# Kernel tuning notes

Measured on AMD Instinct MI355X. Metric: run time of the kernel, lower is better.

## Reference

```python
import jax, jax.numpy as jnp
import numpy as np
from jax import lax

H = 64  # hidden size


def _lstm_layer(x, w_ih, w_hh, b_ih, b_hh):
    """Single LSTM layer, batch_first x: [B, T, D] -> [B, T, H].
    PyTorch gate order: i, f, g, o."""
    B = x.shape[0]
    # Precompute input projections for all timesteps: [T, B, 4H]
    xg = jnp.einsum('btd,gd->tbg', x, w_ih) + (b_ih + b_hh)

    def step(carry, xg_t):
        h, c = carry
        gates = xg_t + h @ w_hh.T  # [B, 4H]
        i, f, g, o = jnp.split(gates, 4, axis=-1)
        i = jax.nn.sigmoid(i)
        f = jax.nn.sigmoid(f)
        g = jnp.tanh(g)
        o = jax.nn.sigmoid(o)
        c = f * c + i * g
        h = o * jnp.tanh(c)
        return (h, c), h

    h0 = jnp.zeros((B, H), dtype=x.dtype)
    c0 = jnp.zeros((B, H), dtype=x.dtype)
    (_, _), hs = lax.scan(step, (h0, c0), xg)  # hs: [T, B, H]
    return jnp.swapaxes(hs, 0, 1)  # [B, T, H]


def setup_inputs() -> dict:
    key = jax.random.key(0)
    ks = jax.random.split(key, 11)
    s = 1.0 / np.sqrt(H)  # PyTorch LSTM init scale
    x = jax.random.normal(ks[0], (8192, 168, 7), dtype=jnp.float32)
    return {
        'x': x,
        'w_ih0': jax.random.normal(ks[1], (4 * H, 7), jnp.float32) * s,
        'w_hh0': jax.random.normal(ks[2], (4 * H, H), jnp.float32) * s,
        'b_ih0': jax.random.normal(ks[3], (4 * H,), jnp.float32) * s,
        'b_hh0': jax.random.normal(ks[4], (4 * H,), jnp.float32) * s,
        'w_ih1': jax.random.normal(ks[5], (4 * H, H), jnp.float32) * s,
        'w_hh1': jax.random.normal(ks[6], (4 * H, H), jnp.float32) * s,
        'b_ih1': jax.random.normal(ks[7], (4 * H,), jnp.float32) * s,
        'b_hh1': jax.random.normal(ks[8], (4 * H,), jnp.float32) * s,
        'fc_w': jax.random.normal(ks[9], (4, H), jnp.float32) * s,
        'fc_b': jax.random.normal(ks[10], (4,), jnp.float32) * s,
    }


def reference(x, w_ih0, w_hh0, b_ih0, b_hh0, w_ih1, w_hh1, b_ih1, b_hh1, fc_w, fc_b):
    h1 = _lstm_layer(x, w_ih0, w_hh0, b_ih0, b_hh0)   # [B, T, H]
    h2 = _lstm_layer(h1, w_ih1, w_hh1, b_ih1, b_hh1)  # [B, T, H]
    last = h2[:, -1, :]                               # dropout is identity in eval
    return last @ fc_w.T + fc_b                       # [B, 4]
```

## Files before the change

kernel.cpp:

```cpp
#include <hip/hip_runtime.h>

#define TT 168
#define HH 64
#define DD 7
#define NS 16
#define BB 8192
#define CH 8
#define NTH 512

typedef float f32x4 __attribute__((ext_vector_type(4)));
typedef _Float16 f16x8 __attribute__((ext_vector_type(8)));

#define MFMA16F(A, B, C) __builtin_amdgcn_mfma_f32_16x16x32_f16((A), (B), (C), 0, 0, 0)

__device__ __forceinline__ f16x8 pack8(f32x4 a, f32x4 b) {
    f16x8 r;
#pragma unroll
    for (int e = 0; e < 4; ++e) { r[e] = (_Float16)a[e]; r[4 + e] = (_Float16)b[e]; }
    return r;
}

__device__ __forceinline__ void cell_update(const f32x4& si, const f32x4& sf,
                                            const f32x4& sg, const f32x4& so,
                                            f32x4& cst, _Float16* dst) {
    f32x4 hv;
#pragma unroll
    for (int r = 0; r < 4; ++r) {
        const float uf = __builtin_amdgcn_exp2f(sf[r]);
        const float fv = __builtin_amdgcn_rcpf(1.0f + uf);
        const float ui = __builtin_amdgcn_exp2f(si[r]);
        const float ug = __builtin_amdgcn_exp2f(fminf(sg[r], 80.0f));
        const float R1 = __builtin_amdgcn_rcpf((1.0f + ui) * (1.0f + ug));
        const float ig = (1.0f - ug) * R1;
        cst[r] = fv * cst[r] + ig;
        const float uo = __builtin_amdgcn_exp2f(so[r]);
        const float uc = __builtin_amdgcn_exp2f(fminf(cst[r] * -2.88539008f, 80.0f));
        const float R2 = __builtin_amdgcn_rcpf((1.0f + uo) * (1.0f + uc));
        hv[r] = (1.0f - uc) * R2;
    }
    unsigned d0, d1;
    asm("v_cvt_pkrtz_f16_f32 %0, %1, %2" : "=v"(d0) : "v"(hv[0]), "v"(hv[1]));
    asm("v_cvt_pkrtz_f16_f32 %0, %1, %2" : "=v"(d1) : "v"(hv[2]), "v"(hv[3]));
    *(uint2*)dst = make_uint2(d0, d1);
}

__global__ __launch_bounds__(NTH, 4)
void weather_lstm_mfma(const float* __restrict__ x,
                       const float* __restrict__ w_ih0, const float* __restrict__ w_hh0,
                       const float* __restrict__ b_ih0, const float* __restrict__ b_hh0,
                       const float* __restrict__ w_ih1, const float* __restrict__ w_hh1,
                       const float* __restrict__ b_ih1, const float* __restrict__ b_hh1,
                       const float* __restrict__ fc_w, const float* __restrict__ fc_b,
                       float* __restrict__ out)
{
    __shared__ f16x8 xs[2][CH][NS];
    __shared__ __align__(16) _Float16 h1[2][NS][72];
    __shared__ __align__(16) _Float16 h2[2][NS][72];

    const int tid  = threadIdx.x;
    const int wv   = tid >> 6;
    const int q    = wv & 3;
    const int lane = tid & 63;
    const int col  = lane & 15;
    const int kg   = lane >> 4;
    const int s0   = blockIdx.x * NS;
    const int ub   = 16 * q + 4 * kg;

    for (int i = tid; i < 2 * NS * 72; i += NTH) {
        ((short*)h1)[i] = 0; ((short*)h2)[i] = 0;
    }
    if (tid < CH * NS) {
        const int tloc = tid >> 4, ss = tid & 15;
        const float* px = x + ((size_t)(s0 + ss) * TT + tloc) * DD;
        f32x4 a, b;
        a[0] = px[0]; a[1] = px[1]; a[2] = px[2]; a[3] = px[3];
        b[0] = px[4]; b[1] = px[5]; b[2] = px[6]; b[3] = 1.0f;
        xs[0][tloc][ss] = pack8(a, b);
    }
    __syncthreads();

    const f16x8 z8 = {0, 0, 0, 0, 0, 0, 0, 0};
    const f32x4 zz = {0, 0, 0, 0};

    if (wv < 4) {
        f16x8 W0[4][2], WX[4];
#pragma unroll
        for (int t4 = 0; t4 < 4; ++t4) {
            const float sc = (t4 == 2) ? -2.88539008f : -1.44269504f;
            const int row = 64 * t4 + 16 * q + col;
#pragma unroll
            for (int kf = 0; kf < 2; ++kf) {
                const float* p = w_hh0 + (size_t)row * HH + 32 * kf + 8 * kg;
                W0[t4][kf] = pack8(*(const f32x4*)p * sc, *(const f32x4*)(p + 4) * sc);
            }
            f32x4 a = {0, 0, 0, 0}, b = {0, 0, 0, 0};
            if (kg == 0) {
                const float* p = w_ih0 + (size_t)row * DD;
                a[0] = p[0]; a[1] = p[1]; a[2] = p[2]; a[3] = p[3];
                b[0] = p[4]; b[1] = p[5]; b[2] = p[6];
                b[3] = b_ih0[row] + b_hh0[row];
            }
            WX[t4] = pack8(a * sc, b * sc);
        }
        f32x4 c1 = {0, 0, 0, 0};

        const f16x8* xbase = &xs[0][0][0];
        const _Float16* r0a = &h1[0][col][8 * kg];
        const _Float16* r0b = &h1[0][col][32 + 8 * kg];
        const _Float16* r1a = &h1[1][col][8 * kg];
        const _Float16* r1b = &h1[1][col][32 + 8 * kg];
        _Float16* wp0 = &h1[0][col][ub];
        _Float16* wp1 = &h1[1][col][ub];

        auto l0_step = [&](const f16x8* xp, const _Float16* ra, const _Float16* rb,
                           _Float16* wr) {
            f32x4 a0, a1, a2, a3;
            __builtin_amdgcn_s_setprio(1);
            f16x8 ax = z8;
            if (kg == 0) ax = *xp;
            a0 = MFMA16F(WX[0], ax, zz);
            a1 = MFMA16F(WX[1], ax, zz);
            a2 = MFMA16F(WX[2], ax, zz);
            a3 = MFMA16F(WX[3], ax, zz);
            f16x8 dh = *(const f16x8*)ra;
            a0 = MFMA16F(W0[0][0], dh, a0);
            a1 = MFMA16F(W0[1][0], dh, a1);
            a2 = MFMA16F(W0[2][0], dh, a2);
            a3 = MFMA16F(W0[3][0], dh, a3);
            dh = *(const f16x8*)rb;
            a0 = MFMA16F(W0[0][1], dh, a0);
            a1 = MFMA16F(W0[1][1], dh, a1);
            a2 = MFMA16F(W0[2][1], dh, a2);
            a3 = MFMA16F(W0[3][1], dh, a3);
            __builtin_amdgcn_s_setprio(0);
            cell_update(a0, a1, a2, a3, c1, wr);
        };
        auto refill = [&](int kref) {
            if (tid < CH * NS) {
                const int tloc = tid >> 4, ss = tid & 15;
                const int tg = kref + CH + tloc;
                const float* px = x + ((size_t)(s0 + ss) * TT + tg) * DD;
                f32x4 a, b;
                a[0] = px[0]; a[1] = px[1]; a[2] = px[2]; a[3] = px[3];
                b[0] = px[4]; b[1] = px[5]; b[2] = px[6]; b[3] = 1.0f;
                const int nb = ((kref >> 3) & 1) ^ 1;
                xs[nb][tloc][ss] = pack8(a, b);
            }
        };

        refill(0);
        l0_step(xbase + col, r1a, r1b, wp0);
        __syncthreads();
        l0_step(xbase + NS + col, r0a, r0b, wp1);
        __syncthreads();

#pragma unroll 1
        for (int j = 1; j < 84; ++j) {
            const f16x8* xpA = xbase + ((2 * j) & 15) * NS + col;
            if ((j & 3) == 0 && j < 80) refill(2 * j);
            l0_step(xpA, r1a, r1b, wp0);
            __syncthreads();
            l0_step(xpA + NS, r0a, r0b, wp1);
            __syncthreads();
        }
        __syncthreads();
    } else {
        f16x8 W1[4][4];
        f32x4 bias1[4];
#pragma unroll
        for (int t4 = 0; t4 < 4; ++t4) {
            const float sc = (t4 == 2) ? -2.88539008f : -1.44269504f;
            const int row = 64 * t4 + 16 * q + col;
            const int rr  = 64 * t4 + 16 * q + 4 * kg;
            bias1[t4] = (*(const f32x4*)(b_ih1 + rr) + *(const f32x4*)(b_hh1 + rr)) * sc;
#pragma unroll
            for (int kf = 0; kf < 4; ++kf) {
                const float* base = (kf < 2) ? (w_ih1 + (size_t)row * HH + 32 * kf)
                                             : (w_hh1 + (size_t)row * HH + 32 * (kf - 2));
                const float* p = base + 8 * kg;
                W1[t4][kf] = pack8(*(const f32x4*)p * sc, *(const f32x4*)(p + 4) * sc);
            }
        }
        f32x4 c2 = {0, 0, 0, 0};

        const _Float16* p1a0 = &h1[0][col][8 * kg];
        const _Float16* p1b0 = &h1[0][col][32 + 8 * kg];
        const _Float16* p1a1 = &h1[1][col][8 * kg];
        const _Float16* p1b1 = &h1[1][col][32 + 8 * kg];
        const _Float16* p2a0 = &h2[0][col][8 * kg];
        const _Float16* p2b0 = &h2[0][col][32 + 8 * kg];
        const _Float16* p2a1 = &h2[1][col][8 * kg];
        const _Float16* p2b1 = &h2[1][col][32 + 8 * kg];
        _Float16* q0 = &h2[0][col][ub];
        _Float16* q1 = &h2[1][col][ub];

        auto l1_step = [&](const _Float16* ha, const _Float16* hb,
                           const _Float16* ea, const _Float16* eb, _Float16* wr) {
            f32x4 a0, a1, a2, a3;
            __builtin_amdgcn_s_setprio(1);
            f16x8 dh = *(const f16x8*)ha;
            a0 = MFMA16F(W1[0][0], dh, bias1[0]);
            a1 = MFMA16F(W1[1][0], dh, bias1[1]);
            a2 = MFMA16F(W1[2][0], dh, bias1[2]);
            a3 = MFMA16F(W1[3][0], dh, bias1[3]);
            dh = *(const f16x8*)hb;
            a0 = MFMA16F(W1[0][1], dh, a0);
            a1 = MFMA16F(W1[1][1], dh, a1);
            a2 = MFMA16F(W1[2][1], dh, a2);
            a3 = MFMA16F(W1[3][1], dh, a3);
            dh = *(const f16x8*)ea;
            a0 = MFMA16F(W1[0][2], dh, a0);
            a1 = MFMA16F(W1[1][2], dh, a1);
            a2 = MFMA16F(W1[2][2], dh, a2);
            a3 = MFMA16F(W1[3][2], dh, a3);
            dh = *(const f16x8*)eb;
            a0 = MFMA16F(W1[0][3], dh, a0);
            a1 = MFMA16F(W1[1][3], dh, a1);
            a2 = MFMA16F(W1[2][3], dh, a2);
            a3 = MFMA16F(W1[3][3], dh, a3);
            __builtin_amdgcn_s_setprio(0);
            cell_update(a0, a1, a2, a3, c2, wr);
        };

        __syncthreads();
        l1_step(p1a0, p1b0, p2a1, p2b1, q0);
        __syncthreads();

#pragma unroll 1
        for (int j = 1; j < 84; ++j) {
            l1_step(p1a1, p1b1, p2a0, p2b0, q1);
            __syncthreads();
            l1_step(p1a0, p1b0, p2a1, p2b1, q0);
            __syncthreads();
        }
        l1_step(p1a1, p1b1, p2a0, p2b0, q1);
        __syncthreads();
    }

    if (tid < NS * 4) {
        const int s = tid >> 2, k = tid & 3;
        float a = fc_b[k];
#pragma unroll
        for (int j = 0; j < HH; ++j)
            a = fmaf((float)h2[1][s][j], fc_w[k * HH + j], a);
        out[(size_t)(s0 + s) * 4 + k] = a;
    }
}

extern "C" void kernel_launch(void* const* d_in, const int* in_sizes, int n_in,
                              void* d_out, int out_size, void* d_ws, size_t ws_size,
                              hipStream_t stream) {
    const float* x     = (const float*)d_in[0];
    const float* w_ih0 = (const float*)d_in[1];
    const float* w_hh0 = (const float*)d_in[2];
    const float* b_ih0 = (const float*)d_in[3];
    const float* b_hh0 = (const float*)d_in[4];
    const float* w_ih1 = (const float*)d_in[5];
    const float* w_hh1 = (const float*)d_in[6];
    const float* b_ih1 = (const float*)d_in[7];
    const float* b_hh1 = (const float*)d_in[8];
    const float* fc_w  = (const float*)d_in[9];
    const float* fc_b  = (const float*)d_in[10];
    float* out = (float*)d_out;

    dim3 grid(BB / NS), block(NTH);
    weather_lstm_mfma<<<grid, block, 0, stream>>>(
        x, w_ih0, w_hh0, b_ih0, b_hh0,
        w_ih1, w_hh1, b_ih1, b_hh1, fc_w, fc_b, out);
}
```

Baseline: 228.2 us.

## Pair cell updates with packed math, drop setprio, zero-padded x buffer

Rewrites the LSTM cell nonlinearity to process two elements at a time with float2 vectors, which permits packed-math instructions. It also merges the forget and input gate reciprocals into one rcp by sharing a denominator, and stores c in a pre-scaled form. The x staging buffer gets a per-kg zero-padded slot so every lane loads unconditionally instead of branching on kg==0. The s_setprio calls around the MFMA sections are removed. The shared-denominator product can overflow or lose precision for large gate inputs, even with exp clamped at 40.

```diff
diff --git a/kernel.cpp b/kernel.cpp
--- a/kernel.cpp
+++ b/kernel.cpp
@@ -8,6 +8,7 @@
 #define CH 8
 #define NTH 512
 
+typedef float f32x2 __attribute__((ext_vector_type(2)));
 typedef float f32x4 __attribute__((ext_vector_type(4)));
 typedef _Float16 f16x8 __attribute__((ext_vector_type(8)));
 
@@ -20,27 +21,43 @@
     return r;
 }
 
-__device__ __forceinline__ void cell_update(const f32x4& si, const f32x4& sf,
-                                            const f32x4& sg, const f32x4& so,
-                                            f32x4& cst, _Float16* dst) {
-    f32x4 hv;
-#pragma unroll
-    for (int r = 0; r < 4; ++r) {
-        const float uf = __builtin_amdgcn_exp2f(sf[r]);
-        const float fv = __builtin_amdgcn_rcpf(1.0f + uf);
-        const float ui = __builtin_amdgcn_exp2f(si[r]);
-        const float ug = __builtin_amdgcn_exp2f(fminf(sg[r], 80.0f));
-        const float R1 = __builtin_amdgcn_rcpf((1.0f + ui) * (1.0f + ug));
-        const float ig = (1.0f - ug) * R1;
-        cst[r] = fv * cst[r] + ig;
-        const float uo = __builtin_amdgcn_exp2f(so[r]);
-        const float uc = __builtin_amdgcn_exp2f(fminf(cst[r] * -2.88539008f, 80.0f));
-        const float R2 = __builtin_amdgcn_rcpf((1.0f + uo) * (1.0f + uc));
-        hv[r] = (1.0f - uc) * R2;
-    }
+__device__ __forceinline__ f32x2 exp2x2(f32x2 a) {
+    return (f32x2){__builtin_amdgcn_exp2f(fminf(a.x, 40.0f)),
+                   __builtin_amdgcn_exp2f(fminf(a.y, 40.0f))};
+}
+__device__ __forceinline__ f32x2 rcpx2(f32x2 a) {
+    return (f32x2){__builtin_amdgcn_rcpf(a.x), __builtin_amdgcn_rcpf(a.y)};
+}
+
+__device__ __forceinline__ void cell_pair(f32x2 si, f32x2 sf, f32x2 sg, f32x2 so,
+                                          f32x2& cs, unsigned& dpk) {
+    const f32x2 one = {1.0f, 1.0f};
+    const f32x2 ui  = exp2x2(si);
+    const f32x2 uf  = exp2x2(sf);
+    const f32x2 ug  = exp2x2(sg);
+    const f32x2 opf = one + uf;
+    const f32x2 pig = (one + ui) * (one + ug);
+    const f32x2 R1  = rcpx2(pig * opf);
+    const f32x2 fv  = pig * R1;
+    const f32x2 igs = (ug * 2.88539008f - (f32x2){2.88539008f, 2.88539008f}) * (opf * R1);
+    cs = fv * cs + igs;
+    const f32x2 uo = exp2x2(so);
+    const f32x2 uc = exp2x2(cs);
+    const f32x2 R2 = rcpx2((one + uo) * (one + uc));
+    const f32x2 hv = (one - uc) * R2;
+    asm("v_cvt_pkrtz_f16_f32 %0, %1, %2" : "=v"(dpk) : "v"(hv.x), "v"(hv.y));
+}
+
+__device__ __forceinline__ void cell_update(const f32x4& gi, const f32x4& gf,
+                                            const f32x4& gg, const f32x4& go,
+                                            f32x4& cs, _Float16* dst) {
+    f32x2 csA = {cs[0], cs[1]}, csB = {cs[2], cs[3]};
     unsigned d0, d1;
-    asm("v_cvt_pkrtz_f16_f32 %0, %1, %2" : "=v"(d0) : "v"(hv[0]), "v"(hv[1]));
-    asm("v_cvt_pkrtz_f16_f32 %0, %1, %2" : "=v"(d1) : "v"(hv[2]), "v"(hv[3]));
+    cell_pair((f32x2){gi[0], gi[1]}, (f32x2){gf[0], gf[1]},
+              (f32x2){gg[0], gg[1]}, (f32x2){go[0], go[1]}, csA, d0);
+    cell_pair((f32x2){gi[2], gi[3]}, (f32x2){gf[2], gf[3]},
+              (f32x2){gg[2], gg[3]}, (f32x2){go[2], go[3]}, csB, d1);
+    cs[0] = csA.x; cs[1] = csA.y; cs[2] = csB.x; cs[3] = csB.y;
     *(uint2*)dst = make_uint2(d0, d1);
 }
 
@@ -53,7 +70,7 @@
                        const float* __restrict__ fc_w, const float* __restrict__ fc_b,
                        float* __restrict__ out)
 {
-    __shared__ f16x8 xs[2][CH][NS];
+    __shared__ f16x8 xs[2][CH][4][NS];
     __shared__ __align__(16) _Float16 h1[2][NS][72];
     __shared__ __align__(16) _Float16 h2[2][NS][72];
 
@@ -69,17 +86,22 @@
     for (int i = tid; i < 2 * NS * 72; i += NTH) {
         ((short*)h1)[i] = 0; ((short*)h2)[i] = 0;
     }
+    {
+        const f16x8 z8i = {0, 0, 0, 0, 0, 0, 0, 0};
+        f16x8* xf = &xs[0][0][0][0];
+        for (int i = tid; i < 2 * CH * 4 * NS; i += NTH) xf[i] = z8i;
+    }
+    __syncthreads();
     if (tid < CH * NS) {
         const int tloc = tid >> 4, ss = tid & 15;
         const float* px = x + ((size_t)(s0 + ss) * TT + tloc) * DD;
         f32x4 a, b;
         a[0] = px[0]; a[1] = px[1]; a[2] = px[2]; a[3] = px[3];
         b[0] = px[4]; b[1] = px[5]; b[2] = px[6]; b[3] = 1.0f;
-        xs[0][tloc][ss] = pack8(a, b);
+        xs[0][tloc][0][ss] = pack8(a, b);
     }
     __syncthreads();
 
-    const f16x8 z8 = {0, 0, 0, 0, 0, 0, 0, 0};
     const f32x4 zz = {0, 0, 0, 0};
 
     if (wv < 4) {
@@ -104,7 +126,7 @@
         }
         f32x4 c1 = {0, 0, 0, 0};
 
-        const f16x8* xbase = &xs[0][0][0];
+        const f16x8* xk = &xs[0][0][kg][col];
         const _Float16* r0a = &h1[0][col][8 * kg];
         const _Float16* r0b = &h1[0][col][32 + 8 * kg];
         const _Float16* r1a = &h1[1][col][8 * kg];
@@ -112,12 +134,10 @@
         _Float16* wp0 = &h1[0][col][ub];
         _Float16* wp1 = &h1[1][col][ub];
 
-        auto l0_step = [&](const f16x8* xp, const _Float16* ra, const _Float16* rb,
+        auto l0_step = [&](int xofs, const _Float16* ra, const _Float16* rb,
                            _Float16* wr) {
             f32x4 a0, a1, a2, a3;
-            __builtin_amdgcn_s_setprio(1);
-            f16x8 ax = z8;
-            if (kg == 0) ax = *xp;
+            const f16x8 ax = xk[xofs];
             a0 = MFMA16F(WX[0], ax, zz);
             a1 = MFMA16F(WX[1], ax, zz);
             a2 = MFMA16F(WX[2], ax, zz);
@@ -132,7 +152,6 @@
             a1 = MFMA16F(W0[1][1], dh, a1);
             a2 = MFMA16F(W0[2][1], dh, a2);
             a3 = MFMA16F(W0[3][1], dh, a3);
-            __builtin_amdgcn_s_setprio(0);
             cell_update(a0, a1, a2, a3, c1, wr);
         };
         auto refill = [&](int kref) {
@@ -144,23 +163,23 @@
                 a[0] = px[0]; a[1] = px[1]; a[2] = px[2]; a[3] = px[3];
                 b[0] = px[4]; b[1] = px[5]; b[2] = px[6]; b[3] = 1.0f;
                 const int nb = ((kref >> 3) & 1) ^ 1;
-                xs[nb][tloc][ss] = pack8(a, b);
+                xs[nb][tloc][0][ss] = pack8(a, b);
             }
         };
 
         refill(0);
-        l0_step(xbase + col, r1a, r1b, wp0);
-        __syncthreads();
-        l0_step(xbase + NS + col, r0a, r0b, wp1);
+        l0_step(0, r1a, r1b, wp0);
+        __syncthreads();
+        l0_step(64, r0a, r0b, wp1);
         __syncthreads();
 
 #pragma unroll 1
         for (int j = 1; j < 84; ++j) {
-            const f16x8* xpA = xbase + ((2 * j) & 15) * NS + col;
+            const int xofs = ((2 * j) & 15) * 64;
             if ((j & 3) == 0 && j < 80) refill(2 * j);
-            l0_step(xpA, r1a, r1b, wp0);
-            __syncthreads();
-            l0_step(xpA + NS, r0a, r0b, wp1);
+            l0_step(xofs, r1a, r1b, wp0);
+            __syncthreads();
+            l0_step(xofs + 64, r0a, r0b, wp1);
             __syncthreads();
         }
         __syncthreads();
@@ -197,7 +216,6 @@
         auto l1_step = [&](const _Float16* ha, const _Float16* hb,
                            const _Float16* ea, const _Float16* eb, _Float16* wr) {
             f32x4 a0, a1, a2, a3;
-            __builtin_amdgcn_s_setprio(1);
             f16x8 dh = *(const f16x8*)ha;
             a0 = MFMA16F(W1[0][0], dh, bias1[0]);
             a1 = MFMA16F(W1[1][0], dh, bias1[1]);
@@ -218,7 +236,6 @@
             a1 = MFMA16F(W1[1][3], dh, a1);
             a2 = MFMA16F(W1[2][3], dh, a2);
             a3 = MFMA16F(W1[3][3], dh, a3);
-            __builtin_amdgcn_s_setprio(0);
             cell_update(a0, a1, a2, a3, c2, wr);
         };
 
```

Measured after the change: 225.8 us. No clear change (-1.0%).
